# Kernel tuning notes

Measured on AMD Instinct MI355X. Metric: run time of the kernel, lower is better.

## Reference

```python
import jax, jax.numpy as jnp
import numpy as np

NUM_CLASSES = 150
FEAT_DIM = 128
N = 1_000_000
TEMPERATURE = 0.15
EPS = 1e-12


def _l2_normalize(x, axis=-1):
    # matches F.normalize(p=2): x / max(||x||, eps)
    n = jnp.sqrt(jnp.sum(x * x, axis=axis, keepdims=True))
    return x / jnp.maximum(n, EPS)


def setup_inputs() -> dict:
    key = jax.random.key(0)
    k1, k2, k3 = jax.random.split(key, 3)
    features = jax.random.normal(k1, (N, FEAT_DIM), dtype=jnp.float32)
    labels = jax.random.randint(k2, (N,), 0, NUM_CLASSES, dtype=jnp.int64)
    # prototypes buffer: random normal, L2-normalized per class (as in _initialize_prototypes)
    prototypes = _l2_normalize(jax.random.normal(k3, (NUM_CLASSES, FEAT_DIM), dtype=jnp.float32))
    return {"features": features, "labels": labels, "prototypes": prototypes}


def reference(features, labels, prototypes):
    # proto_contrastive_loss: normalize, similarity logits, per-sample CE, mean
    f = _l2_normalize(features)                      # [N, D]
    logits = (f @ prototypes.T) / TEMPERATURE        # [N, C]
    logz = jax.nn.logsumexp(logits, axis=-1)         # [N]
    picked = jnp.take_along_axis(logits, labels[:, None].astype(jnp.int32), axis=-1)[:, 0]
    losses = logz - picked                           # cross_entropy, reduction='none'
    return jnp.mean(losses)
```

## Files before the change

kernel.cpp:

```cpp
#include <hip/hip_runtime.h>


#define NS 1000000
#define NC 150
#define NCP 160
#define FD 128
#define NTILE (NS / 16)

static constexpr float INV_T = 1.0f / 0.15f;
static constexpr float MB    = 1.0f / 0.15f;
static constexpr float LOG2E = 1.4426950408889634f;
static constexpr float B2    = -MB * LOG2E;

typedef __attribute__((ext_vector_type(8))) short short8;
typedef __attribute__((ext_vector_type(4))) float f32x4;
typedef unsigned int u32;

#define GLOAD_LDS16(g, l) \
    __builtin_amdgcn_global_load_lds((const __attribute__((address_space(1))) u32*)(g), \
                                     (__attribute__((address_space(3))) u32*)(l), 16, 0, 0)

__device__ __forceinline__ unsigned f2bf_u(float x) {
    unsigned u = __builtin_bit_cast(unsigned, x);
    return (u + 0x7fffu + ((u >> 16) & 1u)) >> 16;
}

__global__ __launch_bounds__(256) void proto_prep(
    const float* __restrict__ protos, u32* __restrict__ dst)
{
    const int tid = threadIdx.x;
#pragma unroll
    for (int i = 0; i < 10; ++i) {
        int c  = i * 256 + tid;
        int r  = c >> 4;
        int cb = c & 15;
        float f[8];
#pragma unroll
        for (int j = 0; j < 8; ++j)
            f[j] = (r < NC) ? protos[r * FD + cb * 8 + j] : 0.0f;
        u32 w[4];
#pragma unroll
        for (int j = 0; j < 4; ++j)
            w[j] = f2bf_u(f[2 * j]) | (f2bf_u(f[2 * j + 1]) << 16);
        u32* out = dst + (r * 64 + ((cb ^ (r & 7)) << 2));
        out[0] = w[0]; out[1] = w[1]; out[2] = w[2]; out[3] = w[3];
    }
}

__global__ __launch_bounds__(256) void proto_ce_mfma(
    const float* __restrict__ feats,
    const int*   __restrict__ labels,
    const u32*   __restrict__ protos_sw,
    double*      __restrict__ partials)
{
    __shared__ __align__(16) char ldsA[NCP * FD * 2];
    __shared__ __align__(16) char ldsF[64 * FD * 4];

    const int tid = threadIdx.x;

    {
        const char* ps = (const char*)protos_sw;
#pragma unroll
        for (int i = 0; i < 10; ++i) {
            int c = i * 256 + tid;
            GLOAD_LDS16(ps + c * 16, ldsA + c * 16);
        }
        const char* fs = (const char*)(feats + (long)blockIdx.x * (64 * FD));
#pragma unroll
        for (int i = 0; i < 8; ++i) {
            int c = i * 256 + tid;
            int r = c >> 5;
            int x = c & 31;
            GLOAD_LDS16(fs + r * 512 + ((x ^ (r & 7)) << 4), ldsF + c * 16);
        }
    }
    __syncthreads();

    const int lane = tid & 63;
    const int wave = tid >> 6;
    const int col  = lane & 15;
    const int grp  = lane >> 4;
    const int gw   = blockIdx.x * 4 + wave;

    const int sw  = (col & 7) << 4;
    const int a0  = col * 256 + ((grp * 16) ^ (sw & 0x30));
    const int ahi = sw & 0x40;

    const int frow = (wave * 16 + col) * 512;
    const int s3   = col & 7;
    const char* f0 = ldsF + frow + (((grp << 1) ^ s3) << 4);
    const char* f1 = ldsF + frow + ((((grp << 1) | 1) ^ s3) << 4);

    const int lrel = -grp * 4;
    const int vcnt = 6 - grp * 4;

    const int lbl = labels[gw * 16 + col];

    f32x4 acc[10];
#pragma unroll
    for (int i = 0; i < 10; ++i) acc[i] = (f32x4){0.f, 0.f, 0.f, 0.f};

    float ssq = 0.0f;
#pragma unroll
    for (int kb = 0; kb < 4; ++kb) {
        float4 A = *(const float4*)(f0 + kb * 128);
        float4 Bv = *(const float4*)(f1 + kb * 128);
        ssq += A.x * A.x + A.y * A.y + A.z * A.z + A.w * A.w;
        ssq += Bv.x * Bv.x + Bv.y * Bv.y + Bv.z * Bv.z + Bv.w * Bv.w;

        short8 bfr;
        bfr[0] = (short)f2bf_u(A.x);  bfr[1] = (short)f2bf_u(A.y);
        bfr[2] = (short)f2bf_u(A.z);  bfr[3] = (short)f2bf_u(A.w);
        bfr[4] = (short)f2bf_u(Bv.x); bfr[5] = (short)f2bf_u(Bv.y);
        bfr[6] = (short)f2bf_u(Bv.z); bfr[7] = (short)f2bf_u(Bv.w);

        const char* ap = ldsA + (a0 + ((kb * 64) ^ ahi));
#pragma unroll
        for (int tt = 0; tt < 10; ++tt) {
            short8 af = *(const short8*)(ap + tt * 4096);
            acc[tt] = __builtin_amdgcn_mfma_f32_16x16x32_bf16(af, bfr, acc[tt], 0, 0, 0);
        }
    }

    ssq += __shfl_xor(ssq, 16, 64);
    ssq += __shfl_xor(ssq, 32, 64);
    const float scl = rsqrtf(fmaxf(ssq, 1e-24f));

    const float k2 = scl * (INV_T * LOG2E);
    const int   lm = lbl + lrel;
    float s0 = 0.f, s1 = 0.f, s2 = 0.f, s3v = 0.f;
    float pick = 0.0f;
#pragma unroll
    for (int tt = 0; tt < 10; ++tt) {
#pragma unroll
        for (int r = 0; r < 4; ++r) {
            float a = acc[tt][r];
            float e = exp2f(fmaf(a, k2, B2));
            if (tt < 9) {
                if      (r == 0) s0 += e;
                else if (r == 1) s1 += e;
                else if (r == 2) s2 += e;
                else             s3v += e;
            } else {
                s0 += (r < vcnt) ? e : 0.0f;
            }
            pick = (tt * 16 + r == lm) ? a : pick;
        }
    }
    float ssum = (s0 + s1) + (s2 + s3v);
    ssum += __shfl_xor(ssum, 16, 64);
    ssum += __shfl_xor(ssum, 32, 64);
    pick += __shfl_xor(pick, 16, 64);
    pick += __shfl_xor(pick, 32, 64);

    float loss = __logf(ssum) + MB - pick * (scl * INV_T);

    loss += __shfl_xor(loss, 1, 64);
    loss += __shfl_xor(loss, 2, 64);
    loss += __shfl_xor(loss, 4, 64);
    loss += __shfl_xor(loss, 8, 64);
    if (lane == 0)
        atomicAdd(&partials[gw & 255], (double)loss);
}

__global__ __launch_bounds__(256) void proto_ce_final(
    const double* __restrict__ partials, float* __restrict__ out)
{
    const int tid = threadIdx.x;
    double v = partials[tid];
#pragma unroll
    for (int off = 32; off > 0; off >>= 1)
        v += __shfl_down(v, off, 64);
    __shared__ double w[4];
    if ((tid & 63) == 0) w[tid >> 6] = v;
    __syncthreads();
    if (tid == 0)
        out[0] = (float)((w[0] + w[1] + w[2] + w[3]) * (1.0 / (double)NS));
}

extern "C" void kernel_launch(void* const* d_in, const int* in_sizes, int n_in,
                              void* d_out, int out_size, void* d_ws, size_t ws_size,
                              hipStream_t stream)
{
    const float* feats  = (const float*)d_in[0];
    const int*   labels = (const int*)d_in[1];
    const float* protos = (const float*)d_in[2];

    u32* protos_sw = (u32*)d_ws;
    double* partials = (double*)((char*)d_ws + NCP * FD * 2);

    (void)hipMemsetAsync(partials, 0, 256 * sizeof(double), stream);
    proto_prep<<<1, 256, 0, stream>>>(protos, protos_sw);
    proto_ce_mfma<<<NS / 64, 256, 0, stream>>>(feats, labels, protos_sw, partials);
    proto_ce_final<<<1, 256, 0, stream>>>(partials, (float*)d_out);
}
```

Baseline: 167.9 us.

## Make CE kernel persistent with double-buffered LDS prefetch of feature tiles

Replaces one-shot 64-row blocks with 256 persistent blocks of 5 waves that loop over 80-row tiles. Each block loads the prototypes into LDS once, then double-buffers feature and label tiles with async global-to-LDS loads so the next tile's load overlaps compute on the current one. This removes the per-block prototype reload and launch overhead. In exchange only 256 blocks run, one per CU given the ~120KB of LDS, which limits occupancy and latency hiding on a bandwidth-bound kernel.

```diff
diff --git a/kernel.cpp b/kernel.cpp
--- a/kernel.cpp
+++ b/kernel.cpp
@@ -5,7 +5,10 @@
 #define NC 150
 #define NCP 160
 #define FD 128
-#define NTILE (NS / 16)
+#define TS 80
+#define NT (NS / TS)
+#define NBLK 256
+#define NTHR 320
 
 static constexpr float INV_T = 1.0f / 0.15f;
 static constexpr float MB    = 1.0f / 0.15f;
@@ -16,7 +19,7 @@
 typedef __attribute__((ext_vector_type(4))) float f32x4;
 typedef unsigned int u32;
 
-#define GLOAD_LDS16(g, l) \
+#define GLOAD16(g, l) \
     __builtin_amdgcn_global_load_lds((const __attribute__((address_space(1))) u32*)(g), \
                                      (__attribute__((address_space(3))) u32*)(l), 16, 0, 0)
 
@@ -47,120 +50,145 @@
     }
 }
 
-__global__ __launch_bounds__(256) void proto_ce_mfma(
+__global__ __launch_bounds__(NTHR) void proto_ce_mfma(
     const float* __restrict__ feats,
     const int*   __restrict__ labels,
     const u32*   __restrict__ protos_sw,
     double*      __restrict__ partials)
 {
-    __shared__ __align__(16) char ldsA[NCP * FD * 2];
-    __shared__ __align__(16) char ldsF[64 * FD * 4];
-
-    const int tid = threadIdx.x;
-
-    {
-        const char* ps = (const char*)protos_sw;
-#pragma unroll
-        for (int i = 0; i < 10; ++i) {
-            int c = i * 256 + tid;
-            GLOAD_LDS16(ps + c * 16, ldsA + c * 16);
-        }
-        const char* fs = (const char*)(feats + (long)blockIdx.x * (64 * FD));
-#pragma unroll
-        for (int i = 0; i < 8; ++i) {
-            int c = i * 256 + tid;
-            int r = c >> 5;
-            int x = c & 31;
-            GLOAD_LDS16(fs + r * 512 + ((x ^ (r & 7)) << 4), ldsF + c * 16);
-        }
-    }
-    __syncthreads();
-
+    __shared__ __align__(16) char lds[123520];
+
+    const int tid  = threadIdx.x;
     const int lane = tid & 63;
     const int wave = tid >> 6;
     const int col  = lane & 15;
     const int grp  = lane >> 4;
-    const int gw   = blockIdx.x * 4 + wave;
+
+    auto stage = [&](int tile, int par) {
+        const char* fs = (const char*)feats + (size_t)tile * (TS * FD * 4);
+        char* fb = lds + 40960 + par * 40960;
+#pragma unroll
+        for (int j = 0; j < 8; ++j) {
+            int c = j * NTHR + tid;
+            int r = c >> 5;
+            int x = c & 31;
+            GLOAD16(fs + r * 512 + ((x ^ (r & 7)) << 4), fb + c * 16);
+        }
+        if (lane < 20)
+            GLOAD16((const char*)labels + (size_t)tile * (TS * 4) + lane * 16,
+                    lds + 122880 + par * 320 + lane * 16);
+    };
+
+    {
+        const char* ps = (const char*)protos_sw;
+#pragma unroll
+        for (int i = 0; i < 8; ++i) {
+            int c = i * NTHR + tid;
+            GLOAD16(ps + c * 16, lds + c * 16);
+        }
+    }
+    stage(blockIdx.x, 0);
+    asm volatile("s_waitcnt vmcnt(0)" ::: "memory");
+    __builtin_amdgcn_s_barrier();
 
     const int sw  = (col & 7) << 4;
     const int a0  = col * 256 + ((grp * 16) ^ (sw & 0x30));
     const int ahi = sw & 0x40;
-
-    const int frow = (wave * 16 + col) * 512;
-    const int s3   = col & 7;
-    const char* f0 = ldsF + frow + (((grp << 1) ^ s3) << 4);
-    const char* f1 = ldsF + frow + ((((grp << 1) | 1) ^ s3) << 4);
-
+    const int s3  = col & 7;
     const int lrel = -grp * 4;
     const int vcnt = 6 - grp * 4;
-
-    const int lbl = labels[gw * 16 + col];
-
-    f32x4 acc[10];
-#pragma unroll
-    for (int i = 0; i < 10; ++i) acc[i] = (f32x4){0.f, 0.f, 0.f, 0.f};
-
-    float ssq = 0.0f;
-#pragma unroll
-    for (int kb = 0; kb < 4; ++kb) {
-        float4 A = *(const float4*)(f0 + kb * 128);
-        float4 Bv = *(const float4*)(f1 + kb * 128);
-        ssq += A.x * A.x + A.y * A.y + A.z * A.z + A.w * A.w;
-        ssq += Bv.x * Bv.x + Bv.y * Bv.y + Bv.z * Bv.z + Bv.w * Bv.w;
-
-        short8 bfr;
-        bfr[0] = (short)f2bf_u(A.x);  bfr[1] = (short)f2bf_u(A.y);
-        bfr[2] = (short)f2bf_u(A.z);  bfr[3] = (short)f2bf_u(A.w);
-        bfr[4] = (short)f2bf_u(Bv.x); bfr[5] = (short)f2bf_u(Bv.y);
-        bfr[6] = (short)f2bf_u(Bv.z); bfr[7] = (short)f2bf_u(Bv.w);
-
-        const char* ap = ldsA + (a0 + ((kb * 64) ^ ahi));
+    const int frow = (wave * 16 + col) * 512;
+
+    float loss_acc = 0.0f;
+    int iter = 0;
+
+    for (int t = blockIdx.x; t < NT; t += NBLK, ++iter) {
+        const int  par  = iter & 1;
+        const bool more = (t + NBLK) < NT;
+
+        if (more) {
+            stage(t + NBLK, par ^ 1);
+            asm volatile("s_waitcnt vmcnt(9)" ::: "memory");
+        } else {
+            asm volatile("s_waitcnt vmcnt(0)" ::: "memory");
+        }
+        __builtin_amdgcn_s_barrier();
+
+        const char* fb = lds + 40960 + par * 40960;
+        const int*  lb = (const int*)(lds + 122880 + par * 320);
+        const char* f0 = fb + frow + (((grp << 1) ^ s3) << 4);
+        const char* f1 = fb + frow + ((((grp << 1) | 1) ^ s3) << 4);
+
+        const int lbl = lb[wave * 16 + col];
+
+        f32x4 acc[10];
+#pragma unroll
+        for (int i = 0; i < 10; ++i) acc[i] = (f32x4){0.f, 0.f, 0.f, 0.f};
+
+        float ssq = 0.0f;
+#pragma unroll
+        for (int kb = 0; kb < 4; ++kb) {
+            float4 A  = *(const float4*)(f0 + kb * 128);
+            float4 Bv = *(const float4*)(f1 + kb * 128);
+            ssq += A.x * A.x + A.y * A.y + A.z * A.z + A.w * A.w;
+            ssq += Bv.x * Bv.x + Bv.y * Bv.y + Bv.z * Bv.z + Bv.w * Bv.w;
+
+            short8 bfr;
+            bfr[0] = (short)f2bf_u(A.x);  bfr[1] = (short)f2bf_u(A.y);
+            bfr[2] = (short)f2bf_u(A.z);  bfr[3] = (short)f2bf_u(A.w);
+            bfr[4] = (short)f2bf_u(Bv.x); bfr[5] = (short)f2bf_u(Bv.y);
+            bfr[6] = (short)f2bf_u(Bv.z); bfr[7] = (short)f2bf_u(Bv.w);
+
+            const char* ap = lds + (a0 + ((kb * 64) ^ ahi));
+#pragma unroll
+            for (int tt = 0; tt < 10; ++tt) {
+                short8 af = *(const short8*)(ap + tt * 4096);
+                acc[tt] = __builtin_amdgcn_mfma_f32_16x16x32_bf16(af, bfr, acc[tt], 0, 0, 0);
+            }
+        }
+
+        ssq += __shfl_xor(ssq, 16, 64);
+        ssq += __shfl_xor(ssq, 32, 64);
+        const float scl = rsqrtf(fmaxf(ssq, 1e-24f));
+
+        const float k2 = scl * (INV_T * LOG2E);
+        const int   lm = lbl + lrel;
+        float s0 = 0.f, s1 = 0.f, s2 = 0.f, s3v = 0.f;
+        float pick = 0.0f;
 #pragma unroll
         for (int tt = 0; tt < 10; ++tt) {
-            short8 af = *(const short8*)(ap + tt * 4096);
-            acc[tt] = __builtin_amdgcn_mfma_f32_16x16x32_bf16(af, bfr, acc[tt], 0, 0, 0);
-        }
+#pragma unroll
+            for (int r = 0; r < 4; ++r) {
+                float a = acc[tt][r];
+                float e = exp2f(fmaf(a, k2, B2));
+                if (tt < 9) {
+                    if      (r == 0) s0 += e;
+                    else if (r == 1) s1 += e;
+                    else if (r == 2) s2 += e;
+                    else             s3v += e;
+                } else {
+                    s0 += (r < vcnt) ? e : 0.0f;
+                }
+                pick = (tt * 16 + r == lm) ? a : pick;
+            }
+        }
+        float ssum = (s0 + s1) + (s2 + s3v);
+        ssum += __shfl_xor(ssum, 16, 64);
+        ssum += __shfl_xor(ssum, 32, 64);
+        pick += __shfl_xor(pick, 16, 64);
+        pick += __shfl_xor(pick, 32, 64);
+
+        loss_acc += __logf(ssum) + MB - pick * (scl * INV_T);
+
+        __builtin_amdgcn_s_barrier();
     }
 
-    ssq += __shfl_xor(ssq, 16, 64);
-    ssq += __shfl_xor(ssq, 32, 64);
-    const float scl = rsqrtf(fmaxf(ssq, 1e-24f));
-
-    const float k2 = scl * (INV_T * LOG2E);
-    const int   lm = lbl + lrel;
-    float s0 = 0.f, s1 = 0.f, s2 = 0.f, s3v = 0.f;
-    float pick = 0.0f;
-#pragma unroll
-    for (int tt = 0; tt < 10; ++tt) {
-#pragma unroll
-        for (int r = 0; r < 4; ++r) {
-            float a = acc[tt][r];
-            float e = exp2f(fmaf(a, k2, B2));
-            if (tt < 9) {
-                if      (r == 0) s0 += e;
-                else if (r == 1) s1 += e;
-                else if (r == 2) s2 += e;
-                else             s3v += e;
-            } else {
-                s0 += (r < vcnt) ? e : 0.0f;
-            }
-            pick = (tt * 16 + r == lm) ? a : pick;
-        }
-    }
-    float ssum = (s0 + s1) + (s2 + s3v);
-    ssum += __shfl_xor(ssum, 16, 64);
-    ssum += __shfl_xor(ssum, 32, 64);
-    pick += __shfl_xor(pick, 16, 64);
-    pick += __shfl_xor(pick, 32, 64);
-
-    float loss = __logf(ssum) + MB - pick * (scl * INV_T);
-
-    loss += __shfl_xor(loss, 1, 64);
-    loss += __shfl_xor(loss, 2, 64);
-    loss += __shfl_xor(loss, 4, 64);
-    loss += __shfl_xor(loss, 8, 64);
+    loss_acc += __shfl_xor(loss_acc, 1, 64);
+    loss_acc += __shfl_xor(loss_acc, 2, 64);
+    loss_acc += __shfl_xor(loss_acc, 4, 64);
+    loss_acc += __shfl_xor(loss_acc, 8, 64);
     if (lane == 0)
-        atomicAdd(&partials[gw & 255], (double)loss);
+        atomicAdd(&partials[(blockIdx.x * 5 + wave) & 255], (double)loss_acc);
 }
 
 __global__ __launch_bounds__(256) void proto_ce_final(
@@ -191,6 +219,6 @@
 
     (void)hipMemsetAsync(partials, 0, 256 * sizeof(double), stream);
     proto_prep<<<1, 256, 0, stream>>>(protos, protos_sw);
-    proto_ce_mfma<<<NS / 64, 256, 0, stream>>>(feats, labels, protos_sw, partials);
+    proto_ce_mfma<<<NBLK, NTHR, 0, stream>>>(feats, labels, protos_sw, partials);
     proto_ce_final<<<1, 256, 0, stream>>>(partials, (float*)d_out);
 }
```

New measurement: 201.0 us. 19.7% more time.
